# Optimization experiments

Measured on AMD Instinct MI355X. Metric: run time of the kernel, lower is better.

Reference implementation:

```python
import jax, jax.numpy as jnp
import numpy as np

SIGMA = 0.1
GAMMA = 1.0 / (SIGMA * SIGMA)  # keops-style gauss kernel: exp(-|x-y|^2 / sigma^2)
B, N, D = 1, 8192, 3


def setup_inputs() -> dict:
    key = jax.random.key(0)
    k1, k2 = jax.random.split(key)
    control_points = jax.random.uniform(k1, (B, N, D), dtype=jnp.float32)
    mom = jax.random.normal(k2, (B, N, D), dtype=jnp.float32) * 0.1
    return {"mom": mom, "control_points": control_points}


def _pairwise_dist2(x, y):
    # x:[B,N,D], y:[B,M,D] -> [B,N,M] squared distances (no N x M x D intermediate)
    x2 = jnp.sum(x * x, -1)  # [B,N]
    y2 = jnp.sum(y * y, -1)  # [B,M]
    xy = jnp.einsum('bnd,bmd->bnm', x, y)
    return x2[:, :, None] + y2[:, None, :] - 2.0 * xy


def gauss_kernel(x, y, b):
    # K(x,y) b : [B,N,d]
    K = jnp.exp(-GAMMA * _pairwise_dist2(x, y))  # [B,N,M]
    return jnp.einsum('bnm,bmd->bnd', K, b)


def gauss_grad_kernel(p, x):
    # dH/dx_i = sum_j d/dx_i[exp(-g|x_i-x_j|^2)] <p_i,p_j>
    #         = -2g * sum_j K_ij <p_i,p_j> (x_i - x_j)
    K = jnp.exp(-GAMMA * _pairwise_dist2(x, x))        # [B,N,N]
    W = K * jnp.einsum('bnd,bmd->bnm', p, p)           # [B,N,N] weighted by <p_i,p_j>
    row_sum = jnp.sum(W, -1)                           # [B,N]
    Wx = jnp.einsum('bnm,bmd->bnd', W, x)              # [B,N,D]
    return (-2.0 * GAMMA) * (x * row_sum[:, :, None] - Wx)


def reference(mom, control_points):
    # variational_evolve: (dp/dt, dx/dt)
    dmom = -gauss_grad_kernel(mom, control_points)
    dx = gauss_kernel(control_points, control_points, mom)
    return (dmom, dx)
```

## Files before the change

kernel.cpp:

```cpp
#include <hip/hip_runtime.h>


#define TPB 256
#define ITILE 4
constexpr float GAMMA_C = 100.0f;
constexpr float LOG2E_C = 1.4426950408889634f;
constexpr float SB_C    = 2.0f * GAMMA_C * LOG2E_C;
constexpr float SC_C    = -GAMMA_C * LOG2E_C;
constexpr float LN2_C   = 0.69314718055994531f;

__global__ __launch_bounds__(TPB, 4) void lddmm_partial(
    const float* __restrict__ mom, const float* __restrict__ xpt,
    float* __restrict__ part, int N, int SEG, int JT) {
  extern __shared__ float4 smem[];
  float4* sA = smem;
  float4* sP = smem + JT;
  const int tid = threadIdx.x;
  const int seg = blockIdx.y;

  for (int t = tid; t < JT; t += TPB) {
    const int j = seg * JT + t;
    const float bx = xpt[3*j], by = xpt[3*j+1], bz = xpt[3*j+2];
    sA[t] = make_float4(SB_C*bx, SB_C*by, SB_C*bz,
                        SC_C * fmaf(bx, bx, fmaf(by, by, bz*bz)));
    sP[t] = make_float4(mom[3*j], mom[3*j+1], mom[3*j+2], 0.f);
  }
  __syncthreads();

  const int i0 = blockIdx.x * (TPB * ITILE) + tid;

  float xi[ITILE], yi[ITILE], zi[ITILE];
  float px[ITILE], py[ITILE], pz[ITILE], ci[ITILE];
#pragma unroll
  for (int u = 0; u < ITILE; ++u) {
    const int i = i0 + u * TPB;
    xi[u] = xpt[3*i]; yi[u] = xpt[3*i+1]; zi[u] = xpt[3*i+2];
    px[u] = mom[3*i]; py[u] = mom[3*i+1]; pz[u] = mom[3*i+2];
    ci[u] = SC_C * fmaf(xi[u], xi[u], fmaf(yi[u], yi[u], zi[u]*zi[u]));
  }

  float a[ITILE], wx[ITILE], wy[ITILE], wz[ITILE];
  float gx[ITILE], gy[ITILE], gz[ITILE];
#pragma unroll
  for (int u = 0; u < ITILE; ++u) {
    a[u]=0.f; wx[u]=0.f; wy[u]=0.f; wz[u]=0.f;
    gx[u]=0.f; gy[u]=0.f; gz[u]=0.f;
  }

#pragma unroll 2
  for (int t = 0; t < JT; ++t) {
    const float4 A = sA[t];
    const float4 P = sP[t];
#pragma unroll
    for (int u = 0; u < ITILE; ++u) {
      const float arg = fmaf(A.x, xi[u],
                        fmaf(A.y, yi[u],
                        fmaf(A.z, zi[u], ci[u] + A.w)));
      const float K   = __builtin_amdgcn_exp2f(arg);
      const float dot = fmaf(P.x, px[u], fmaf(P.y, py[u], P.z * pz[u]));
      const float w   = K * dot;
      a[u] += w;
      wx[u] = fmaf(w, A.x, wx[u]);
      wy[u] = fmaf(w, A.y, wy[u]);
      wz[u] = fmaf(w, A.z, wz[u]);
      gx[u] = fmaf(K, P.x, gx[u]);
      gy[u] = fmaf(K, P.y, gy[u]);
      gz[u] = fmaf(K, P.z, gz[u]);
    }
  }

  const size_t SN = (size_t)SEG * N;
  float* p = part + (size_t)seg * N;
#pragma unroll
  for (int u = 0; u < ITILE; ++u) {
    const int i = i0 + u * TPB;
    p[0*SN+i] = a[u];
    p[1*SN+i] = wx[u];
    p[2*SN+i] = wy[u];
    p[3*SN+i] = wz[u];
    p[4*SN+i] = gx[u];
    p[5*SN+i] = gy[u];
    p[6*SN+i] = gz[u];
  }
}

__global__ __launch_bounds__(TPB) void lddmm_reduce(
    const float* __restrict__ part, float* __restrict__ R, int N, int SEG) {
  const int i = blockIdx.x * TPB + threadIdx.x;
  const int c = blockIdx.y;
  const float* src = part + (size_t)c * SEG * N + i;
  float s0 = 0.f, s1 = 0.f, s2 = 0.f, s3 = 0.f;
  int s = 0;
  for (; s + 4 <= SEG; s += 4) {
    s0 += src[(size_t)(s+0)*N]; s1 += src[(size_t)(s+1)*N];
    s2 += src[(size_t)(s+2)*N]; s3 += src[(size_t)(s+3)*N];
  }
  for (; s < SEG; ++s) s0 += src[(size_t)s*N];
  R[(size_t)c * N + i] = (s0 + s1) + (s2 + s3);
}

__global__ __launch_bounds__(TPB) void lddmm_finalize(
    const float* __restrict__ R, const float* __restrict__ xpt,
    float* __restrict__ out, int N) {
  const int i = blockIdx.x * TPB + threadIdx.x;
  const float A  = R[i];
  const float WX = R[(size_t)1*N+i], WY = R[(size_t)2*N+i], WZ = R[(size_t)3*N+i];
  const float GX = R[(size_t)4*N+i], GY = R[(size_t)5*N+i], GZ = R[(size_t)6*N+i];
  const float xi = xpt[3*i], yi = xpt[3*i+1], zi = xpt[3*i+2];
  const float TGA = 2.0f * GAMMA_C * A;
  out[3*i+0] = fmaf(TGA, xi, -LN2_C * WX);
  out[3*i+1] = fmaf(TGA, yi, -LN2_C * WY);
  out[3*i+2] = fmaf(TGA, zi, -LN2_C * WZ);
  out[3*N + 3*i + 0] = GX;
  out[3*N + 3*i + 1] = GY;
  out[3*N + 3*i + 2] = GZ;
}

__global__ __launch_bounds__(TPB) void lddmm_atomic(
    const float* __restrict__ mom, const float* __restrict__ xpt,
    float* __restrict__ out, int N) {
  const int i  = blockIdx.x * TPB + threadIdx.x;
  const int jb = blockIdx.y * TPB;
  __shared__ float4 sA[TPB], sP[TPB];
  {
    const int j = jb + threadIdx.x;
    const float bx = xpt[3*j], by = xpt[3*j+1], bz = xpt[3*j+2];
    sA[threadIdx.x] = make_float4(SB_C*bx, SB_C*by, SB_C*bz,
                                  SC_C * fmaf(bx, bx, fmaf(by, by, bz*bz)));
    sP[threadIdx.x] = make_float4(mom[3*j], mom[3*j+1], mom[3*j+2], 0.f);
  }
  __syncthreads();
  const float xi = xpt[3*i], yi = xpt[3*i+1], zi = xpt[3*i+2];
  const float pxi = mom[3*i], pyi = mom[3*i+1], pzi = mom[3*i+2];
  const float ci = SC_C * fmaf(xi, xi, fmaf(yi, yi, zi*zi));
  float a=0.f, wx=0.f, wy=0.f, wz=0.f, gx=0.f, gy=0.f, gz=0.f;
#pragma unroll 4
  for (int t = 0; t < TPB; ++t) {
    const float4 A = sA[t], P = sP[t];
    const float arg = fmaf(A.x, xi, fmaf(A.y, yi, fmaf(A.z, zi, ci + A.w)));
    const float K   = __builtin_amdgcn_exp2f(arg);
    const float dot = fmaf(P.x, pxi, fmaf(P.y, pyi, P.z * pzi));
    const float w   = K * dot;
    a += w;
    wx = fmaf(w, A.x, wx); wy = fmaf(w, A.y, wy); wz = fmaf(w, A.z, wz);
    gx = fmaf(K, P.x, gx); gy = fmaf(K, P.y, gy); gz = fmaf(K, P.z, gz);
  }
  const float TGA = 2.0f * GAMMA_C * a;
  atomicAdd(&out[3*i+0], fmaf(TGA, xi, -LN2_C * wx));
  atomicAdd(&out[3*i+1], fmaf(TGA, yi, -LN2_C * wy));
  atomicAdd(&out[3*i+2], fmaf(TGA, zi, -LN2_C * wz));
  atomicAdd(&out[3*N+3*i+0], gx);
  atomicAdd(&out[3*N+3*i+1], gy);
  atomicAdd(&out[3*N+3*i+2], gz);
}

extern "C" void kernel_launch(void* const* d_in, const int* in_sizes, int n_in,
                              void* d_out, int out_size, void* d_ws, size_t ws_size,
                              hipStream_t stream) {
  const float* mom = (const float*)d_in[0];
  const float* xpt = (const float*)d_in[1];
  float* out = (float*)d_out;
  const int N = in_sizes[0] / 3;

  auto need = [&](int s) { return (size_t)(7*s + 7) * (size_t)N * sizeof(float); };
  int SEG = 128;
  while (SEG > 2 && need(SEG) > ws_size) SEG >>= 1;

  const bool shapes_ok = (N % (TPB * ITILE) == 0) && (N % SEG == 0) &&
                         ((N / SEG) <= TPB);
  if (need(SEG) <= ws_size && shapes_ok) {
    const int JT = N / SEG;
    float* partb = (float*)d_ws;
    float* R     = partb + (size_t)7 * SEG * N;
    const size_t shmem = (size_t)JT * 2 * sizeof(float4);
    dim3 gA(N / (TPB * ITILE), SEG);
    lddmm_partial<<<gA, TPB, shmem, stream>>>(mom, xpt, partb, N, SEG, JT);
    dim3 gB(N / TPB, 7);
    lddmm_reduce<<<gB, TPB, 0, stream>>>(partb, R, N, SEG);
    lddmm_finalize<<<N / TPB, TPB, 0, stream>>>(R, xpt, out, N);
  } else {
    hipMemsetAsync(d_out, 0, (size_t)out_size * sizeof(float), stream);
    dim3 grid(N / TPB, N / TPB);
    lddmm_atomic<<<grid, TPB, 0, stream>>>(mom, xpt, out, N);
  }
}
```

Before: 99.54 us.

## Use packed FP32 math over j-pairs with a precomputed SoA-paired source layout

Adds a prep kernel that precomputes scaled source coordinates, norms and momenta into a j-pair interleaved layout. The partial kernel now runs two j columns per lane with v_pk_fma/v_pk_mul/v_pk_add, roughly halving the VALU instruction count for the non-exp work, while ITILE drops from 4 to 2. This costs an extra kernel launch, more workspace, and a horizontal add of the packed accumulators at the end. The exp2 calls stay scalar, so the transcendental unit remains a possible bottleneck.

```diff
diff --git a/kernel.cpp b/kernel.cpp
--- a/kernel.cpp
+++ b/kernel.cpp
@@ -2,70 +2,114 @@
 
 
 #define TPB 256
-#define ITILE 4
+#define ITILE 2
 constexpr float GAMMA_C = 100.0f;
 constexpr float LOG2E_C = 1.4426950408889634f;
 constexpr float SB_C    = 2.0f * GAMMA_C * LOG2E_C;
 constexpr float SC_C    = -GAMMA_C * LOG2E_C;
 constexpr float LN2_C   = 0.69314718055994531f;
 
+typedef float v2f __attribute__((ext_vector_type(2)));
+
+static __device__ __forceinline__ v2f pk_fma(v2f a, v2f b, v2f c) {
+  v2f d;
+  asm("v_pk_fma_f32 %0, %1, %2, %3" : "=v"(d) : "v"(a), "v"(b), "v"(c));
+  return d;
+}
+static __device__ __forceinline__ v2f pk_mul(v2f a, v2f b) {
+  v2f d;
+  asm("v_pk_mul_f32 %0, %1, %2" : "=v"(d) : "v"(a), "v"(b));
+  return d;
+}
+static __device__ __forceinline__ v2f pk_add(v2f a, v2f b) {
+  v2f d;
+  asm("v_pk_add_f32 %0, %1, %2" : "=v"(d) : "v"(a), "v"(b));
+  return d;
+}
+
+__global__ __launch_bounds__(TPB) void lddmm_prep(
+    const float* __restrict__ mom, const float* __restrict__ xpt,
+    float4* __restrict__ J2, int N) {
+  const int jp = blockIdx.x * TPB + threadIdx.x;
+  if (jp >= N / 2) return;
+  const int j0 = 2 * jp, j1 = 2 * jp + 1;
+  const float x0 = xpt[3*j0], y0 = xpt[3*j0+1], z0 = xpt[3*j0+2];
+  const float x1 = xpt[3*j1], y1 = xpt[3*j1+1], z1 = xpt[3*j1+2];
+  const float n0 = SC_C * fmaf(x0, x0, fmaf(y0, y0, z0*z0));
+  const float n1 = SC_C * fmaf(x1, x1, fmaf(y1, y1, z1*z1));
+  J2[4*jp+0] = make_float4(SB_C*x0, SB_C*x1, SB_C*y0, SB_C*y1);
+  J2[4*jp+1] = make_float4(SB_C*z0, SB_C*z1, n0, n1);
+  J2[4*jp+2] = make_float4(mom[3*j0], mom[3*j1], mom[3*j0+1], mom[3*j1+1]);
+  J2[4*jp+3] = make_float4(mom[3*j0+2], mom[3*j1+2], 0.f, 0.f);
+}
+
 __global__ __launch_bounds__(TPB, 4) void lddmm_partial(
     const float* __restrict__ mom, const float* __restrict__ xpt,
+    const float4* __restrict__ J2,
     float* __restrict__ part, int N, int SEG, int JT) {
-  extern __shared__ float4 smem[];
-  float4* sA = smem;
-  float4* sP = smem + JT;
+  extern __shared__ float4 sL[];
   const int tid = threadIdx.x;
   const int seg = blockIdx.y;
-
-  for (int t = tid; t < JT; t += TPB) {
-    const int j = seg * JT + t;
-    const float bx = xpt[3*j], by = xpt[3*j+1], bz = xpt[3*j+2];
-    sA[t] = make_float4(SB_C*bx, SB_C*by, SB_C*bz,
-                        SC_C * fmaf(bx, bx, fmaf(by, by, bz*bz)));
-    sP[t] = make_float4(mom[3*j], mom[3*j+1], mom[3*j+2], 0.f);
-  }
+  const int JP = JT / 2;
+
+  for (int t = tid; t < JP * 4; t += TPB)
+    sL[t] = J2[(size_t)seg * JP * 4 + t];
   __syncthreads();
 
   const int i0 = blockIdx.x * (TPB * ITILE) + tid;
 
-  float xi[ITILE], yi[ITILE], zi[ITILE];
-  float px[ITILE], py[ITILE], pz[ITILE], ci[ITILE];
+  v2f X[ITILE], Y[ITILE], Z[ITILE], C[ITILE];
+  v2f PX[ITILE], PY[ITILE], PZ[ITILE];
 #pragma unroll
   for (int u = 0; u < ITILE; ++u) {
     const int i = i0 + u * TPB;
-    xi[u] = xpt[3*i]; yi[u] = xpt[3*i+1]; zi[u] = xpt[3*i+2];
-    px[u] = mom[3*i]; py[u] = mom[3*i+1]; pz[u] = mom[3*i+2];
-    ci[u] = SC_C * fmaf(xi[u], xi[u], fmaf(yi[u], yi[u], zi[u]*zi[u]));
-  }
-
-  float a[ITILE], wx[ITILE], wy[ITILE], wz[ITILE];
-  float gx[ITILE], gy[ITILE], gz[ITILE];
+    const float x = xpt[3*i], y = xpt[3*i+1], z = xpt[3*i+2];
+    const float px = mom[3*i], py = mom[3*i+1], pz = mom[3*i+2];
+    const float c = SC_C * fmaf(x, x, fmaf(y, y, z*z));
+    X[u] = (v2f){x, x};  Y[u] = (v2f){y, y};  Z[u] = (v2f){z, z};
+    C[u] = (v2f){c, c};
+    PX[u] = (v2f){px, px}; PY[u] = (v2f){py, py}; PZ[u] = (v2f){pz, pz};
+  }
+
+  v2f aA[ITILE], aWX[ITILE], aWY[ITILE], aWZ[ITILE];
+  v2f aGX[ITILE], aGY[ITILE], aGZ[ITILE];
 #pragma unroll
   for (int u = 0; u < ITILE; ++u) {
-    a[u]=0.f; wx[u]=0.f; wy[u]=0.f; wz[u]=0.f;
-    gx[u]=0.f; gy[u]=0.f; gz[u]=0.f;
+    aA[u] = (v2f){0.f, 0.f};
+    aWX[u] = (v2f){0.f, 0.f}; aWY[u] = (v2f){0.f, 0.f}; aWZ[u] = (v2f){0.f, 0.f};
+    aGX[u] = (v2f){0.f, 0.f}; aGY[u] = (v2f){0.f, 0.f}; aGZ[u] = (v2f){0.f, 0.f};
   }
 
 #pragma unroll 2
-  for (int t = 0; t < JT; ++t) {
-    const float4 A = sA[t];
-    const float4 P = sP[t];
+  for (int pp = 0; pp < JP; ++pp) {
+    const float4 q0 = sL[4*pp+0];
+    const float4 q1 = sL[4*pp+1];
+    const float4 q2 = sL[4*pp+2];
+    const float4 q3 = sL[4*pp+3];
+    const v2f Ax = (v2f){q0.x, q0.y}, Ay = (v2f){q0.z, q0.w};
+    const v2f Az = (v2f){q1.x, q1.y}, Aw = (v2f){q1.z, q1.w};
+    const v2f Px = (v2f){q2.x, q2.y}, Py = (v2f){q2.z, q2.w};
+    const v2f Pz = (v2f){q3.x, q3.y};
 #pragma unroll
     for (int u = 0; u < ITILE; ++u) {
-      const float arg = fmaf(A.x, xi[u],
-                        fmaf(A.y, yi[u],
-                        fmaf(A.z, zi[u], ci[u] + A.w)));
-      const float K   = __builtin_amdgcn_exp2f(arg);
-      const float dot = fmaf(P.x, px[u], fmaf(P.y, py[u], P.z * pz[u]));
-      const float w   = K * dot;
-      a[u] += w;
-      wx[u] = fmaf(w, A.x, wx[u]);
-      wy[u] = fmaf(w, A.y, wy[u]);
-      wz[u] = fmaf(w, A.z, wz[u]);
-      gx[u] = fmaf(K, P.x, gx[u]);
-      gy[u] = fmaf(K, P.y, gy[u]);
-      gz[u] = fmaf(K, P.z, gz[u]);
+      v2f t = pk_fma(Az, Z[u], Aw);
+      t = pk_fma(Ay, Y[u], t);
+      t = pk_fma(Ax, X[u], t);
+      const v2f arg = pk_add(t, C[u]);
+      v2f K;
+      K.x = __builtin_amdgcn_exp2f(arg.x);
+      K.y = __builtin_amdgcn_exp2f(arg.y);
+      v2f d = pk_mul(Pz, PZ[u]);
+      d = pk_fma(Py, PY[u], d);
+      d = pk_fma(Px, PX[u], d);
+      const v2f w = pk_mul(K, d);
+      aA[u]  = pk_add(aA[u], w);
+      aWX[u] = pk_fma(w, Ax, aWX[u]);
+      aWY[u] = pk_fma(w, Ay, aWY[u]);
+      aWZ[u] = pk_fma(w, Az, aWZ[u]);
+      aGX[u] = pk_fma(K, Px, aGX[u]);
+      aGY[u] = pk_fma(K, Py, aGY[u]);
+      aGZ[u] = pk_fma(K, Pz, aGZ[u]);
     }
   }
 
@@ -74,13 +118,13 @@
 #pragma unroll
   for (int u = 0; u < ITILE; ++u) {
     const int i = i0 + u * TPB;
-    p[0*SN+i] = a[u];
-    p[1*SN+i] = wx[u];
-    p[2*SN+i] = wy[u];
-    p[3*SN+i] = wz[u];
-    p[4*SN+i] = gx[u];
-    p[5*SN+i] = gy[u];
-    p[6*SN+i] = gz[u];
+    p[0*SN+i] = aA[u].x  + aA[u].y;
+    p[1*SN+i] = aWX[u].x + aWX[u].y;
+    p[2*SN+i] = aWY[u].x + aWY[u].y;
+    p[3*SN+i] = aWZ[u].x + aWZ[u].y;
+    p[4*SN+i] = aGX[u].x + aGX[u].y;
+    p[5*SN+i] = aGY[u].x + aGY[u].y;
+    p[6*SN+i] = aGZ[u].x + aGZ[u].y;
   }
 }
 
@@ -162,19 +206,22 @@
   float* out = (float*)d_out;
   const int N = in_sizes[0] / 3;
 
-  auto need = [&](int s) { return (size_t)(7*s + 7) * (size_t)N * sizeof(float); };
+  auto need = [&](int s) { return (size_t)(8 + 7*s + 7) * (size_t)N * sizeof(float); };
   int SEG = 128;
   while (SEG > 2 && need(SEG) > ws_size) SEG >>= 1;
 
+  const int JT = N / SEG;
   const bool shapes_ok = (N % (TPB * ITILE) == 0) && (N % SEG == 0) &&
-                         ((N / SEG) <= TPB);
+                         (JT % 2 == 0) && (N % 2 == 0);
   if (need(SEG) <= ws_size && shapes_ok) {
-    const int JT = N / SEG;
-    float* partb = (float*)d_ws;
+    const int JP = JT / 2;
+    float4* J2   = (float4*)d_ws;
+    float* partb = (float*)d_ws + (size_t)8 * N;
     float* R     = partb + (size_t)7 * SEG * N;
-    const size_t shmem = (size_t)JT * 2 * sizeof(float4);
+    lddmm_prep<<<(N/2 + TPB - 1) / TPB, TPB, 0, stream>>>(mom, xpt, J2, N);
+    const size_t shmem = (size_t)JP * 4 * sizeof(float4);
     dim3 gA(N / (TPB * ITILE), SEG);
-    lddmm_partial<<<gA, TPB, shmem, stream>>>(mom, xpt, partb, N, SEG, JT);
+    lddmm_partial<<<gA, TPB, shmem, stream>>>(mom, xpt, J2, partb, N, SEG, JT);
     dim3 gB(N / TPB, 7);
     lddmm_reduce<<<gB, TPB, 0, stream>>>(partb, R, N, SEG);
     lddmm_finalize<<<N / TPB, TPB, 0, stream>>>(R, xpt, out, N);
```

New measurement: 100.9 us. About the same (+1.3%).
